# Performance work log

Hardware: AMD Instinct MI355X
Metric: run time of the kernel (lower is better)

The kernel has to match this reference:

```python
import jax, jax.numpy as jnp
import numpy as np

EPS = 1e-12  # matches torch F.normalize default eps


def setup_inputs() -> dict:
    key = jax.random.key(0)
    img_feats = jax.random.normal(key, (8192, 1024), dtype=jnp.float32)
    return {"img_feats": img_feats}


def reference(img_feats):
    # L2-normalize along feature dim (torch F.normalize: x / max(||x||, eps))
    norm = jnp.maximum(jnp.linalg.norm(img_feats, axis=-1, keepdims=True), EPS)
    feats_n = img_feats / norm                       # [N, D]
    sims = feats_n @ feats_n.T                        # [N, N] cosine similarities
    # mask self-similarity on the diagonal with -inf
    n = sims.shape[0]
    diag = jnp.arange(n)
    sims = sims.at[diag, diag].set(-jnp.inf)
    attn_weights = jax.nn.softmax(sims, axis=-1)      # [N, N]
    out = attn_weights @ img_feats                    # [N, D]
    return out, attn_weights
```

## Files before the change

### kernel.cpp

```cpp
#include <hip/hip_runtime.h>
#include <hip/hip_bf16.h>
#include <stdint.h>

#define NR 8192
#define ND 1024

typedef __attribute__((ext_vector_type(8))) short bf16x8;
typedef __attribute__((ext_vector_type(4))) float f32x4;
typedef __attribute__((ext_vector_type(4))) float fvec4;
typedef __attribute__((ext_vector_type(8))) unsigned short u16x8;

static __device__ __forceinline__ uint16_t f2bf(float f) {
  union { __hip_bfloat16 h; uint16_t u; } cv;
  cv.h = __float2bfloat16(f);
  return cv.u;
}
static __device__ __forceinline__ float bf2f(uint16_t u) {
  union { uint32_t i; float f; } cv;
  cv.i = ((uint32_t)u) << 16;
  return cv.f;
}

__global__ void k_norm(const float* __restrict__ X, uint16_t* __restrict__ Xn) {
  const int row = blockIdx.x;
  const int t = threadIdx.x;
  const float4 v = reinterpret_cast<const float4*>(X + (size_t)row * ND)[t];
  float ss = v.x * v.x + v.y * v.y + v.z * v.z + v.w * v.w;
#pragma unroll
  for (int m = 1; m < 64; m <<= 1) ss += __shfl_xor(ss, m, 64);
  __shared__ float sred[4];
  if ((t & 63) == 0) sred[t >> 6] = ss;
  __syncthreads();
  const float tot = sred[0] + sred[1] + sred[2] + sred[3];
  const float inv = 1.0f / fmaxf(sqrtf(tot), 1e-12f);
  ushort4 o;
  o.x = f2bf(v.x * inv); o.y = f2bf(v.y * inv);
  o.z = f2bf(v.z * inv); o.w = f2bf(v.w * inv);
  reinterpret_cast<ushort4*>(Xn + (size_t)row * ND)[t] = o;
}

__global__ void k_transpose(const float* __restrict__ X, uint16_t* __restrict__ XT) {
  __shared__ uint16_t tile[32][33];
  const int ntr = NR / 32;
  const int bx = blockIdx.x % ntr;
  const int by = blockIdx.x / ntr;
  const int r0 = bx * 32, d0 = by * 32;
  const int t = threadIdx.x;
  const int rr = t >> 3, cc = (t & 7) * 4;
  const float4 v = *reinterpret_cast<const float4*>(&X[(size_t)(r0 + rr) * ND + d0 + cc]);
  tile[cc + 0][rr] = f2bf(v.x);
  tile[cc + 1][rr] = f2bf(v.y);
  tile[cc + 2][rr] = f2bf(v.z);
  tile[cc + 3][rr] = f2bf(v.w);
  __syncthreads();
  ushort4 o;
  o.x = tile[rr][cc + 0]; o.y = tile[rr][cc + 1];
  o.z = tile[rr][cc + 2]; o.w = tile[rr][cc + 3];
  *reinterpret_cast<ushort4*>(&XT[(size_t)(d0 + rr) * NR + r0 + cc]) = o;
}

template <int MH, int NH>
static __device__ __forceinline__ void mfma16(f32x4 (&acc)[8][4],
                                              const bf16x8 (&a_)[4][2],
                                              const bf16x8 (&b_)[2][2]) {
  __builtin_amdgcn_s_setprio(1);
#pragma unroll
  for (int kk = 0; kk < 2; ++kk)
#pragma unroll
    for (int m4 = 0; m4 < 4; ++m4)
#pragma unroll
      for (int n2 = 0; n2 < 2; ++n2)
        acc[MH * 4 + m4][NH * 2 + n2] = __builtin_amdgcn_mfma_f32_16x16x32_bf16(
            a_[m4][kk], b_[n2][kk], acc[MH * 4 + m4][NH * 2 + n2], 0, 0, 0);
  __builtin_amdgcn_s_setprio(0);
}

#define BAR()    __builtin_amdgcn_s_barrier()
#define LGKM()   asm volatile("s_waitcnt lgkmcnt(0)" ::: "memory")
#define VMW4()   asm volatile("s_waitcnt vmcnt(4)" ::: "memory")
#define VMW0()   asm volatile("s_waitcnt vmcnt(0)" ::: "memory")
#define SCHED0() __builtin_amdgcn_sched_barrier(0)

template <int EPI, int NKT>
static __device__ __forceinline__ void gemm8_core(
    char* sm,
    const uint16_t* __restrict__ A, int lda,
    const uint16_t* __restrict__ B, int ldb,
    int row0, int col0,
    float* __restrict__ C, int ldc,
    uint16_t* __restrict__ Eo, float* __restrict__ partials, int rb, int cb) {
  const int tid = threadIdx.x;
  const int wid = tid >> 6;
  const int lane = tid & 63;
  const int wr = wid >> 2;
  const int wc = wid & 3;
  const int flane = lane & 15;
  const int qw = lane >> 4;
  const int rkey = flane & 7;
  const int rowb = flane * 128;

  const int colb = (((tid & 7) ^ ((tid >> 3) & 7)) * 16);
  const int r0s = tid >> 3;

  const char* const Abyte = (const char*)A + (size_t)row0 * lda * 2;
  const char* const Bbyte = (const char*)B + (size_t)col0 * ldb * 2;

  f32x4 acc[8][4] = {};
  bf16x8 a_[4][2], b_[2][2];

  auto stageH = [&](int d, int isB, int h, int t) {
    const char* gb = isB ? Bbyte : Abyte;
    const int ld2 = (isB ? ldb : lda) * 2;
    const char* g0 = gb + (size_t)(h * 128 + r0s) * ld2 + t * 128 + colb;
    const char* g1 = g0 + (size_t)64 * ld2;
    char* l0 = sm + d * 65536 + isB * 32768 + h * 16384 + (wid << 10);
    __builtin_amdgcn_global_load_lds((const __attribute__((address_space(1))) void*)g0,
                                     (__attribute__((address_space(3))) void*)l0, 16, 0, 0);
    __builtin_amdgcn_global_load_lds((const __attribute__((address_space(1))) void*)g1,
                                     (__attribute__((address_space(3))) void*)(l0 + 8192), 16, 0, 0);
  };
  auto rdA = [&](int d, int mhalf) {
#pragma unroll
    for (int m4 = 0; m4 < 4; ++m4)
#pragma unroll
      for (int kk = 0; kk < 2; ++kk) {
        const int chunk = (qw + kk * 4) ^ rkey;
        a_[m4][kk] = *(const bf16x8*)(sm + d * 65536 + wr * 16384 +
                                      (mhalf * 4 + m4) * 2048 + rowb + chunk * 16);
      }
  };
  auto rdB = [&](int d, int nhalf) {
#pragma unroll
    for (int n2 = 0; n2 < 2; ++n2)
#pragma unroll
      for (int kk = 0; kk < 2; ++kk) {
        const int chunk = (qw + kk * 4) ^ rkey;
        b_[n2][kk] = *(const bf16x8*)(sm + d * 65536 + 32768 + (wc >> 1) * 16384 +
                                      (wc & 1) * 8192 + (nhalf * 2 + n2) * 2048 +
                                      rowb + chunk * 16);
      }
  };

  stageH(0, 0, 0, 0); stageH(0, 0, 1, 0); stageH(0, 1, 0, 0); stageH(0, 1, 1, 0);
  stageH(1, 0, 0, 1); stageH(1, 0, 1, 1);
  VMW4();
  BAR();

  const int niter = NKT / 2;
  for (int i = 0; i < niter; ++i) {
    const int t0 = 2 * i, t1 = t0 + 1;
    const bool s0 = (t0 + 2 < NKT), s1 = (t1 + 2 < NKT);
    rdA(0, 0); rdB(0, 0);
    stageH(1, 1, 0, t1); stageH(1, 1, 1, t1);
    BAR(); LGKM(); SCHED0(); mfma16<0, 0>(acc, a_, b_); BAR();
    rdB(0, 1);
    BAR(); LGKM(); SCHED0(); mfma16<0, 1>(acc, a_, b_); BAR();
    rdA(0, 1);
    BAR(); LGKM(); SCHED0(); mfma16<1, 1>(acc, a_, b_); BAR();
    rdB(0, 0);
    if (s0) { stageH(0, 0, 0, t0 + 2); stageH(0, 0, 1, t0 + 2); }
    BAR(); LGKM(); SCHED0(); mfma16<1, 0>(acc, a_, b_);
    if (s0) { VMW4(); } else { VMW0(); }
    BAR();
    rdA(1, 0); rdB(1, 0);
    if (s0) { stageH(0, 1, 0, t0 + 2); stageH(0, 1, 1, t0 + 2); }
    BAR(); LGKM(); SCHED0(); mfma16<0, 0>(acc, a_, b_); BAR();
    rdB(1, 1);
    BAR(); LGKM(); SCHED0(); mfma16<0, 1>(acc, a_, b_); BAR();
    rdA(1, 1);
    BAR(); LGKM(); SCHED0(); mfma16<1, 1>(acc, a_, b_); BAR();
    rdB(1, 0);
    if (s1) { stageH(1, 0, 0, t1 + 2); stageH(1, 0, 1, t1 + 2); }
    BAR(); LGKM(); SCHED0(); mfma16<1, 0>(acc, a_, b_);
    if (s1) { VMW4(); } else if (s0) { VMW0(); }
    BAR();
  }

  const int e0 = (lane >> 4) * 4;

  if constexpr (EPI == 0) {
    const bool diag = (rb == cb);
    float rp[8][4] = {};
    float rpT[4] = {};
#pragma unroll
    for (int m = 0; m < 8; ++m) {
      const int growb = row0 + wr * 128 + m * 16 + e0;
#pragma unroll
      for (int n = 0; n < 4; ++n) {
        const int gcol = col0 + wc * 64 + n * 16 + flane;
        ushort4 mpack;
#pragma unroll
        for (int e = 0; e < 4; ++e) {
          const int grow = growb + e;
          const float ev = (grow == gcol) ? 0.0f : __expf(acc[m][n][e]);
          const uint16_t eb = f2bf(ev);
          const float evr = bf2f(eb);
          Eo[(size_t)grow * NR + gcol] = eb;
          rp[m][e] += evr;
          rpT[n] += evr;
          ((uint16_t*)&mpack)[e] = eb;
        }
        if (!diag) {
          const int mr = wc * 64 + n * 16 + flane;
          const int mc = wr * 128 + m * 16 + e0;
          int byte = mr * 512 + mc * 2;
          byte ^= (mr & 7) << 4;
          *reinterpret_cast<ushort4*>(sm + byte) = mpack;
        }
      }
    }
#pragma unroll
    for (int msk = 1; msk <= 8; msk <<= 1)
#pragma unroll
      for (int m = 0; m < 8; ++m)
#pragma unroll
        for (int e = 0; e < 4; ++e) rp[m][e] += __shfl_xor(rp[m][e], msk, 64);
#pragma unroll
    for (int msk = 16; msk <= 32; msk <<= 1)
#pragma unroll
      for (int n = 0; n < 4; ++n) rpT[n] += __shfl_xor(rpT[n], msk, 64);

    __syncthreads();
    if (!diag) {
#pragma unroll
      for (int p = 0; p < 16; ++p) {
        const int mr = p * 16 + (tid >> 5);
        const int ch = tid & 31;
        int byte = mr * 512 + ch * 16;
        byte ^= (mr & 7) << 4;
        const u16x8 v = *reinterpret_cast<const u16x8*>(sm + byte);
        *reinterpret_cast<u16x8*>(&Eo[(size_t)(col0 + mr) * NR + row0 + ch * 8]) = v;
      }
    }
    __syncthreads();

    float* sRow = (float*)sm;
    float* sCol = (float*)(sm + 4096);
    if (flane == 0) {
#pragma unroll
      for (int m = 0; m < 8; ++m)
#pragma unroll
        for (int e = 0; e < 4; ++e)
          sRow[wc * 256 + wr * 128 + m * 16 + e0 + e] = rp[m][e];
    }
    if (lane < 16) {
#pragma unroll
      for (int n = 0; n < 4; ++n) sCol[wr * 256 + wc * 64 + n * 16 + lane] = rpT[n];
    }
    __syncthreads();
    if (tid < 256) {
      partials[(size_t)cb * NR + row0 + tid] =
          sRow[tid] + sRow[256 + tid] + sRow[512 + tid] + sRow[768 + tid];
      if (!diag)
        partials[(size_t)rb * NR + col0 + tid] = sCol[tid] + sCol[256 + tid];
    }
  } else {
#pragma unroll
    for (int m = 0; m < 8; ++m)
#pragma unroll
      for (int n = 0; n < 4; ++n)
#pragma unroll
        for (int e = 0; e < 4; ++e)
          C[(size_t)(row0 + wr * 128 + m * 16 + e0 + e) * ldc +
            col0 + wc * 64 + n * 16 + flane] = acc[m][n][e];
  }
}

__global__ __launch_bounds__(512, 2) void k_gemm_sym8(
    const uint16_t* __restrict__ Xn, uint16_t* __restrict__ E,
    float* __restrict__ partials) {
  extern __shared__ char smem[];
  const int nwg = gridDim.x;
  const int cpx = nwg >> 3;
  const int b = blockIdx.x;
  const int swz = (b & 7) * cpx + (b >> 3);
  int rem = swz, rb = 0;
  while (rem >= 32 - rb) { rem -= 32 - rb; ++rb; }
  const int cb = rb + rem;
  gemm8_core<0, 16>(smem, Xn, ND, Xn, ND, rb * 256, cb * 256,
                    nullptr, 0, E, partials, rb, cb);
}

__global__ __launch_bounds__(512, 2) void k_gemm_pv8(
    const uint16_t* __restrict__ E, const uint16_t* __restrict__ XT,
    float* __restrict__ P) {
  extern __shared__ char smem[];
  const int b = blockIdx.x;
  const int swz = (b & 7) * 32 + (b >> 3);
  const int s = swz >> 7;
  const int t = swz & 127;
  const int by = t >> 2, bx = t & 3;
  gemm8_core<1, 64>(smem, E + (size_t)s * 4096, NR, XT + (size_t)s * 4096, NR,
                    by * 256, bx * 256, P + (size_t)s * NR * ND, ND,
                    nullptr, nullptr, 0, 0);
}

__global__ void k_rowsum(const float* __restrict__ partials, float* __restrict__ rowsum,
                         int ncb) {
  const int r = blockIdx.x * blockDim.x + threadIdx.x;
  float s = 0.0f;
  for (int cb = 0; cb < ncb; ++cb) s += partials[(size_t)cb * NR + r];
  rowsum[r] = s;
}

__global__ void k_fixup(const fvec4* __restrict__ P0, const fvec4* __restrict__ P1,
                        const float* __restrict__ rowsum, fvec4* __restrict__ out) {
  const size_t i = (size_t)blockIdx.x * blockDim.x + threadIdx.x;
  const int row = (int)(i >> 8);
  const float inv = 1.0f / rowsum[row];
  const fvec4 a = __builtin_nontemporal_load(&P0[i]);
  const fvec4 b = __builtin_nontemporal_load(&P1[i]);
  const fvec4 o = (a + b) * inv;
  __builtin_nontemporal_store(o, &out[i]);
}

__global__ void k_scale(const uint16_t* __restrict__ E, const float* __restrict__ rowsum,
                        float* __restrict__ attn) {
  const size_t total = (size_t)NR * NR / 8;
  for (size_t i = (size_t)blockIdx.x * blockDim.x + threadIdx.x; i < total;
       i += (size_t)gridDim.x * blockDim.x) {
    const int row = (int)(i >> 10);
    const float inv = 1.0f / rowsum[row];
    const u16x8 e = reinterpret_cast<const u16x8*>(E)[i];
    fvec4 o0, o1;
    o0.x = bf2f(e[0]) * inv; o0.y = bf2f(e[1]) * inv;
    o0.z = bf2f(e[2]) * inv; o0.w = bf2f(e[3]) * inv;
    o1.x = bf2f(e[4]) * inv; o1.y = bf2f(e[5]) * inv;
    o1.z = bf2f(e[6]) * inv; o1.w = bf2f(e[7]) * inv;
    __builtin_nontemporal_store(o0, &reinterpret_cast<fvec4*>(attn)[2 * i + 0]);
    __builtin_nontemporal_store(o1, &reinterpret_cast<fvec4*>(attn)[2 * i + 1]);
  }
}

extern "C" void kernel_launch(void* const* d_in, const int* in_sizes, int n_in,
                              void* d_out, int out_size, void* d_ws, size_t ws_size,
                              hipStream_t stream) {
  const float* X = (const float*)d_in[0];
  float* out = (float*)d_out;
  float* attn = out + (size_t)NR * ND;

  char* ws = (char*)d_ws;
  const size_t off_Xn   = 0;
  const size_t off_XT   = off_Xn + (size_t)NR * ND * 2;
  const size_t off_E    = off_XT + (size_t)ND * NR * 2;
  const size_t off_part = off_E + (size_t)NR * NR * 2;
  const size_t off_rs   = off_part + (size_t)64 * NR * 4;
  const size_t needed   = off_rs + (size_t)NR * 4;
  if (ws_size < needed) return;

  uint16_t* Xn  = (uint16_t*)(ws + off_Xn);
  uint16_t* XT  = (uint16_t*)(ws + off_XT);
  uint16_t* E   = (uint16_t*)(ws + off_E);
  float* partials = (float*)(ws + off_part);
  float* rowsum   = (float*)(ws + off_rs);

  float* P = attn;

  (void)hipFuncSetAttribute((const void*)k_gemm_sym8,
                            hipFuncAttributeMaxDynamicSharedMemorySize, 131072);
  (void)hipFuncSetAttribute((const void*)k_gemm_pv8,
                            hipFuncAttributeMaxDynamicSharedMemorySize, 131072);

  k_norm<<<NR, 256, 0, stream>>>(X, Xn);
  k_transpose<<<(NR / 32) * (ND / 32), 256, 0, stream>>>(X, XT);
  k_gemm_sym8<<<528, 512, 131072, stream>>>(Xn, E, partials);
  k_rowsum<<<NR / 256, 256, 0, stream>>>(partials, rowsum, 32);
  k_gemm_pv8<<<256, 512, 131072, stream>>>(E, XT, P);
  k_fixup<<<NR * ND / 4 / 256, 256, 0, stream>>>(
      (const fvec4*)P, (const fvec4*)(P + (size_t)NR * ND), rowsum, (fvec4*)out);
  k_scale<<<2048, 256, 0, stream>>>(E, rowsum, attn);
}
```

Measured before the change: 377.1 us.

## Fuse attention-weight normalization into PV GEMM tile loads, drop scale kernel

Removes the separate k_scale pass that re-read the bf16 exp matrix E and wrote fp32 attention weights. Instead, each PV GEMM workgroup writes its share of the A tiles already staged in LDS, scaled by the precomputed inverse row sums, so E is read only once. The split-K partials move from the attn output buffer into a dedicated workspace region, and k_rowsum now stores reciprocals. The trade-off is extra stores and barriers inside the GEMM main loop for one column-group of workgroups, which can create load imbalance and stall the MFMA pipeline, plus a larger workspace requirement.

Result: faster. 303.6 us (-19.5%).

```diff
diff --git a/kernel.cpp b/kernel.cpp
--- a/kernel.cpp
+++ b/kernel.cpp
@@ -88,7 +88,8 @@
     const uint16_t* __restrict__ B, int ldb,
     int row0, int col0,
     float* __restrict__ C, int ldc,
-    uint16_t* __restrict__ Eo, float* __restrict__ partials, int rb, int cb) {
+    uint16_t* __restrict__ Eo, float* __restrict__ partials, int rb, int cb,
+    float* __restrict__ emitA, const float* __restrict__ invrs, int bx_emit) {
   const int tid = threadIdx.x;
   const int wid = tid >> 6;
   const int lane = tid & 63;
@@ -107,6 +108,15 @@
 
   f32x4 acc[8][4] = {};
   bf16x8 a_[4][2], b_[2][2];
+
+  float invr0 = 0, invr1 = 0, invr2 = 0, invr3 = 0;
+  if constexpr (EPI == 1) {
+    const int rb0 = tid >> 3;
+    invr0 = invrs[row0 + rb0];
+    invr1 = invrs[row0 + 64 + rb0];
+    invr2 = invrs[row0 + 128 + rb0];
+    invr3 = invrs[row0 + 192 + rb0];
+  }
 
   auto stageH = [&](int d, int isB, int h, int t) {
     const char* gb = isB ? Bbyte : Abyte;
@@ -140,6 +150,25 @@
                                       rowb + chunk * 16);
       }
   };
+  auto emitT = [&](int d, int t) {
+    const int c8 = tid & 7;
+    const int rbase = tid >> 3;
+#pragma unroll
+    for (int p = 0; p < 4; ++p) {
+      const int r = p * 64 + rbase;
+      const u16x8 ev = *(const u16x8*)(sm + d * 65536 + ((r >> 7) * 16384) +
+                                       (r & 127) * 128 + ((c8 ^ (r & 7)) << 4));
+      const float inv = (p == 0) ? invr0 : (p == 1) ? invr1 : (p == 2) ? invr2 : invr3;
+      fvec4 o0, o1;
+      o0.x = bf2f(ev[0]) * inv; o0.y = bf2f(ev[1]) * inv;
+      o0.z = bf2f(ev[2]) * inv; o0.w = bf2f(ev[3]) * inv;
+      o1.x = bf2f(ev[4]) * inv; o1.y = bf2f(ev[5]) * inv;
+      o1.z = bf2f(ev[6]) * inv; o1.w = bf2f(ev[7]) * inv;
+      float* dst = emitA + (size_t)(row0 + r) * NR + t * 64 + c8 * 8;
+      __builtin_nontemporal_store(o0, (fvec4*)dst);
+      __builtin_nontemporal_store(o1, (fvec4*)(dst + 4));
+    }
+  };
 
   stageH(0, 0, 0, 0); stageH(0, 0, 1, 0); stageH(0, 1, 0, 0); stageH(0, 1, 1, 0);
   stageH(1, 0, 0, 1); stageH(1, 0, 1, 1);
@@ -150,6 +179,7 @@
   for (int i = 0; i < niter; ++i) {
     const int t0 = 2 * i, t1 = t0 + 1;
     const bool s0 = (t0 + 2 < NKT), s1 = (t1 + 2 < NKT);
+    const bool doEmit = (EPI == 1) && ((t0 >> 4) == bx_emit);
     rdA(0, 0); rdB(0, 0);
     stageH(1, 1, 0, t1); stageH(1, 1, 1, t1);
     BAR(); LGKM(); SCHED0(); mfma16<0, 0>(acc, a_, b_); BAR();
@@ -157,6 +187,9 @@
     BAR(); LGKM(); SCHED0(); mfma16<0, 1>(acc, a_, b_); BAR();
     rdA(0, 1);
     BAR(); LGKM(); SCHED0(); mfma16<1, 1>(acc, a_, b_); BAR();
+    if constexpr (EPI == 1) {
+      if (doEmit) { emitT(0, t0); LGKM(); BAR(); }
+    }
     rdB(0, 0);
     if (s0) { stageH(0, 0, 0, t0 + 2); stageH(0, 0, 1, t0 + 2); }
     BAR(); LGKM(); SCHED0(); mfma16<1, 0>(acc, a_, b_);
@@ -169,6 +202,9 @@
     BAR(); LGKM(); SCHED0(); mfma16<0, 1>(acc, a_, b_); BAR();
     rdA(1, 1);
     BAR(); LGKM(); SCHED0(); mfma16<1, 1>(acc, a_, b_); BAR();
+    if constexpr (EPI == 1) {
+      if (doEmit) { emitT(1, t1); LGKM(); BAR(); }
+    }
     rdB(1, 0);
     if (s1) { stageH(1, 0, 0, t1 + 2); stageH(1, 0, 1, t1 + 2); }
     BAR(); LGKM(); SCHED0(); mfma16<1, 0>(acc, a_, b_);
@@ -278,12 +314,13 @@
   while (rem >= 32 - rb) { rem -= 32 - rb; ++rb; }
   const int cb = rb + rem;
   gemm8_core<0, 16>(smem, Xn, ND, Xn, ND, rb * 256, cb * 256,
-                    nullptr, 0, E, partials, rb, cb);
+                    nullptr, 0, E, partials, rb, cb, nullptr, nullptr, -1);
 }
 
 __global__ __launch_bounds__(512, 2) void k_gemm_pv8(
     const uint16_t* __restrict__ E, const uint16_t* __restrict__ XT,
-    float* __restrict__ P) {
+    float* __restrict__ P, float* __restrict__ attn,
+    const float* __restrict__ invrs) {
   extern __shared__ char smem[];
   const int b = blockIdx.x;
   const int swz = (b & 7) * 32 + (b >> 3);
@@ -292,7 +329,8 @@
   const int by = t >> 2, bx = t & 3;
   gemm8_core<1, 64>(smem, E + (size_t)s * 4096, NR, XT + (size_t)s * 4096, NR,
                     by * 256, bx * 256, P + (size_t)s * NR * ND, ND,
-                    nullptr, nullptr, 0, 0);
+                    nullptr, nullptr, 0, 0,
+                    attn + (size_t)s * 4096, invrs, bx);
 }
 
 __global__ void k_rowsum(const float* __restrict__ partials, float* __restrict__ rowsum,
@@ -300,36 +338,18 @@
   const int r = blockIdx.x * blockDim.x + threadIdx.x;
   float s = 0.0f;
   for (int cb = 0; cb < ncb; ++cb) s += partials[(size_t)cb * NR + r];
-  rowsum[r] = s;
+  rowsum[r] = 1.0f / s;
 }
 
 __global__ void k_fixup(const fvec4* __restrict__ P0, const fvec4* __restrict__ P1,
                         const float* __restrict__ rowsum, fvec4* __restrict__ out) {
   const size_t i = (size_t)blockIdx.x * blockDim.x + threadIdx.x;
   const int row = (int)(i >> 8);
-  const float inv = 1.0f / rowsum[row];
+  const float inv = rowsum[row];
   const fvec4 a = __builtin_nontemporal_load(&P0[i]);
   const fvec4 b = __builtin_nontemporal_load(&P1[i]);
   const fvec4 o = (a + b) * inv;
   __builtin_nontemporal_store(o, &out[i]);
-}
-
-__global__ void k_scale(const uint16_t* __restrict__ E, const float* __restrict__ rowsum,
-                        float* __restrict__ attn) {
-  const size_t total = (size_t)NR * NR / 8;
-  for (size_t i = (size_t)blockIdx.x * blockDim.x + threadIdx.x; i < total;
-       i += (size_t)gridDim.x * blockDim.x) {
-    const int row = (int)(i >> 10);
-    const float inv = 1.0f / rowsum[row];
-    const u16x8 e = reinterpret_cast<const u16x8*>(E)[i];
-    fvec4 o0, o1;
-    o0.x = bf2f(e[0]) * inv; o0.y = bf2f(e[1]) * inv;
-    o0.z = bf2f(e[2]) * inv; o0.w = bf2f(e[3]) * inv;
-    o1.x = bf2f(e[4]) * inv; o1.y = bf2f(e[5]) * inv;
-    o1.z = bf2f(e[6]) * inv; o1.w = bf2f(e[7]) * inv;
-    __builtin_nontemporal_store(o0, &reinterpret_cast<fvec4*>(attn)[2 * i + 0]);
-    __builtin_nontemporal_store(o1, &reinterpret_cast<fvec4*>(attn)[2 * i + 1]);
-  }
 }
 
 extern "C" void kernel_launch(void* const* d_in, const int* in_sizes, int n_in,
@@ -345,7 +365,8 @@
   const size_t off_E    = off_XT + (size_t)ND * NR * 2;
   const size_t off_part = off_E + (size_t)NR * NR * 2;
   const size_t off_rs   = off_part + (size_t)64 * NR * 4;
-  const size_t needed   = off_rs + (size_t)NR * 4;
+  const size_t off_P    = off_rs + (size_t)NR * 4;
+  const size_t needed   = off_P + (size_t)2 * NR * ND * 4;
   if (ws_size < needed) return;
 
   uint16_t* Xn  = (uint16_t*)(ws + off_Xn);
@@ -353,8 +374,7 @@
   uint16_t* E   = (uint16_t*)(ws + off_E);
   float* partials = (float*)(ws + off_part);
   float* rowsum   = (float*)(ws + off_rs);
-
-  float* P = attn;
+  float* P        = (float*)(ws + off_P);
 
   (void)hipFuncSetAttribute((const void*)k_gemm_sym8,
                             hipFuncAttributeMaxDynamicSharedMemorySize, 131072);
@@ -365,8 +385,7 @@
   k_transpose<<<(NR / 32) * (ND / 32), 256, 0, stream>>>(X, XT);
   k_gemm_sym8<<<528, 512, 131072, stream>>>(Xn, E, partials);
   k_rowsum<<<NR / 256, 256, 0, stream>>>(partials, rowsum, 32);
-  k_gemm_pv8<<<256, 512, 131072, stream>>>(E, XT, P);
+  k_gemm_pv8<<<256, 512, 131072, stream>>>(E, XT, P, attn, rowsum);
   k_fixup<<<NR * ND / 4 / 256, 256, 0, stream>>>(
       (const fvec4*)P, (const fvec4*)(P + (size_t)NR * ND), rowsum, (fvec4*)out);
-  k_scale<<<2048, 256, 0, stream>>>(E, rowsum, attn);
-}
+}
```
